# Optimization experiments

Hardware: AMD Instinct MI355X
Metric: run time of the kernel (lower is better)

## Reference

```python
import jax, jax.numpy as jnp
import numpy as np

N, E, D = 100000, 1280000, 64


def setup_inputs() -> dict:
    key = jax.random.key(0)
    ks = jax.random.split(key, 9)
    x = jax.random.normal(ks[0], (N, D), jnp.float32)
    edge_index = jax.random.randint(ks[1], (2, E), 0, N, dtype=jnp.int64)
    edge_weight = jax.random.uniform(ks[2], (E,), jnp.float32)
    s = 1.0 / np.sqrt(D)
    W0 = jax.random.normal(ks[3], (D, D), jnp.float32) * s
    b0 = jnp.zeros((D,), jnp.float32)
    W1 = jax.random.normal(ks[4], (D, D), jnp.float32) * s
    b1 = jnp.zeros((D,), jnp.float32)
    W2 = jax.random.normal(ks[5], (D, D), jnp.float32) * s
    b2 = jnp.zeros((D,), jnp.float32)
    return {"x": x, "edge_index": edge_index, "edge_weight": edge_weight,
            "W0": W0, "b0": b0, "W1": W1, "b1": b1, "W2": W2, "b2": b2}


def reference(x, edge_index, edge_weight, W0, b0, W1, b1, W2, b2):
    n = x.shape[0]
    row, col = edge_index[0], edge_index[1]
    # GCN normalization with self-loops (PyG gcn_norm, fill_value=1)
    loop = jnp.arange(n)
    row_f = jnp.concatenate([row, loop])
    col_f = jnp.concatenate([col, loop])
    w_f = jnp.concatenate([edge_weight, jnp.ones((n,), x.dtype)])
    deg = jax.ops.segment_sum(w_f, col_f, num_segments=n)
    dinv = jnp.where(deg > 0, jax.lax.rsqrt(deg), 0.0).astype(x.dtype)
    norm = dinv[row_f] * w_f * dinv[col_f]  # [E+N]

    def conv(h, W, b):
        h = h @ W                                  # [N, D_out]
        msg = h[row_f] * norm[:, None]             # gather + scale
        return jax.ops.segment_sum(msg, col_f, num_segments=n) + b

    results = [x]
    h = jax.nn.relu(conv(x, W0, b0))   # dropout p=0 / eval -> identity
    results.append(h)
    h = jax.nn.relu(conv(h, W1, b1))
    results.append(h)
    h = conv(h, W2, b2)                # last layer: no activation
    results.append(h)
    return tuple(results)
```

## Files before the change

kernel.cpp:

```cpp
#include <hip/hip_runtime.h>


#define TPB 256
#define P1_CHUNK 8192
#define DSH 7
#define DNB 128
#define STAGE_CAP 4096

__global__ __launch_bounds__(TPB) void k_p0(const int* __restrict__ col,
                                            int* __restrict__ chist, int E, int nbk) {
    __shared__ int h[1024];
    int tid = threadIdx.x;
    for (int i = tid; i < nbk; i += TPB) h[i] = 0;
    __syncthreads();
    int s0 = blockIdx.x * P1_CHUNK;
    int s1 = min(s0 + P1_CHUNK, E);
    for (int i = s0 + tid; i < s1; i += TPB) atomicAdd(&h[col[i] >> DSH], 1);
    __syncthreads();
    for (int i = tid; i < nbk; i += TPB)
        if (h[i]) atomicAdd(&chist[i], h[i]);
}

__global__ __launch_bounds__(1024) void k_scanb(const int* __restrict__ chist,
                                                int* __restrict__ cbase,
                                                int* __restrict__ ccur, int nbk, int E) {
    __shared__ int s[1024];
    int tid = threadIdx.x;
    int v = (tid < nbk) ? chist[tid] : 0;
    s[tid] = v;
    __syncthreads();
    for (int off = 1; off < 1024; off <<= 1) {
        int t = (tid >= off) ? s[tid - off] : 0;
        __syncthreads();
        s[tid] += t;
        __syncthreads();
    }
    if (tid < nbk) { int ex = s[tid] - v; cbase[tid] = ex; ccur[tid] = ex; }
    if (tid == 0) cbase[nbk] = E;
}

__global__ __launch_bounds__(TPB) void k_p1(const int* __restrict__ row,
                                            const int* __restrict__ col,
                                            const float* __restrict__ w,
                                            int* __restrict__ ccur,
                                            int2* __restrict__ bkt, int E, int nbk) {
    __shared__ int h[1024];
    __shared__ int base[1024];
    int tid = threadIdx.x;
    for (int i = tid; i < nbk; i += TPB) h[i] = 0;
    __syncthreads();
    int s0 = blockIdx.x * P1_CHUNK;
    int s1 = min(s0 + P1_CHUNK, E);
    for (int i = s0 + tid; i < s1; i += TPB) atomicAdd(&h[col[i] >> DSH], 1);
    __syncthreads();
    for (int i = tid; i < nbk; i += TPB) {
        int c = h[i];
        base[i] = c ? atomicAdd(&ccur[i], c) : 0;
        h[i] = 0;
    }
    __syncthreads();
    for (int i = s0 + tid; i < s1; i += TPB) {
        int c = col[i];
        int b = c >> DSH;
        int r = atomicAdd(&h[b], 1);
        bkt[base[b] + r] = make_int2(row[i] | ((c & (DNB - 1)) << 20), __float_as_int(w[i]));
    }
}

__global__ __launch_bounds__(TPB) void k_p2(const int2* __restrict__ bkt,
                                            const int* __restrict__ cbase,
                                            int* __restrict__ starts,
                                            int2* __restrict__ edges,
                                            float* __restrict__ dinv, int n, int E) {
    __shared__ int hist[DNB];
    __shared__ int curs[DNB];
    __shared__ int sc[DNB];
    __shared__ int2 stage[STAGE_CAP];
    int tid = threadIdx.x;
    int b = blockIdx.x;
    int s0 = cbase[b], s1 = cbase[b + 1];
    int cnt = s1 - s0;
    int nodeBase = b << DSH;
    if (tid < DNB) hist[tid] = 0;
    __syncthreads();
    for (int i = s0 + tid; i < s1; i += TPB)
        atomicAdd(&hist[(unsigned)bkt[i].x >> 20], 1);
    __syncthreads();
    int v = 0;
    if (tid < DNB) { v = hist[tid]; sc[tid] = v; }
    __syncthreads();
    for (int off = 1; off < DNB; off <<= 1) {
        int t = 0;
        if (tid < DNB && tid >= off) t = sc[tid - off];
        __syncthreads();
        if (tid < DNB) sc[tid] += t;
        __syncthreads();
    }
    if (tid < DNB) {
        int ex = sc[tid] - v;
        curs[tid] = ex;
        int node = nodeBase + tid;
        if (node < n) starts[node] = s0 + ex;
    }
    if (b == 0 && tid == 0) starts[n] = E;
    __syncthreads();
    if (cnt <= STAGE_CAP) {
        for (int i = s0 + tid; i < s1; i += TPB) {
            int2 ed = bkt[i];
            int d = (unsigned)ed.x >> 20;
            int r = atomicAdd(&curs[d], 1);
            stage[r] = make_int2(ed.x & 0xFFFFF, ed.y);
        }
        __syncthreads();
        for (int i = tid; i < cnt; i += TPB) edges[s0 + i] = stage[i];
        if (tid < DNB) {
            int node = nodeBase + tid;
            if (node < n) {
                float d = 1.0f;
                for (int j = sc[tid] - v; j < sc[tid]; ++j)
                    d += __int_as_float(stage[j].y);
                dinv[node] = rsqrtf(d);
            }
        }
    } else {
        for (int i = s0 + tid; i < s1; i += TPB) {
            int2 ed = bkt[i];
            int d = (unsigned)ed.x >> 20;
            int r = atomicAdd(&curs[d], 1);
            edges[s0 + r] = make_int2(ed.x & 0xFFFFF, ed.y);
        }
        __syncthreads();
        if (tid < DNB) {
            int node = nodeBase + tid;
            if (node < n) {
                float d = 1.0f;
                for (int j = sc[tid] - v; j < sc[tid]; ++j)
                    d += __int_as_float(edges[s0 + j].y);
                dinv[node] = rsqrtf(d);
            }
        }
    }
}

__global__ __launch_bounds__(TPB, 3) void k_gemm64(const float* __restrict__ in,
                                                   const float* __restrict__ Wg,
                                                   float* __restrict__ out,
                                                   float* __restrict__ cp, int n) {
    __shared__ float4 Ws[1024];
    __shared__ float4 As[2048];
    int tid = threadIdx.x;
    const float4* Wf4 = (const float4*)Wg;
    #pragma unroll
    for (int i = 0; i < 4; ++i) Ws[i * 256 + tid] = Wf4[i * 256 + tid];
    int rowbase = blockIdx.x * 128;
    const float4* Af4 = (const float4*)in;
    #pragma unroll
    for (int i = 0; i < 8; ++i) {
        int f4 = i * 256 + tid;
        int r = f4 >> 4, c4 = f4 & 15;
        float4 v = make_float4(0.f, 0.f, 0.f, 0.f);
        if (rowbase + r < n) {
            v = Af4[(size_t)(rowbase + r) * 16 + c4];
            if (cp) *(float4*)&cp[((size_t)(rowbase + r) * 16 + c4) * 4] = v;
        }
        As[r * 16 + (c4 ^ ((r >> 3) & 3))] = v;
    }
    __syncthreads();
    int jg = tid & 15;
    int rg = tid >> 4;
    int r0 = rg * 8;
    int sw = rg & 3;
    float4 acc[8];
    #pragma unroll
    for (int rr = 0; rr < 8; ++rr) acc[rr] = make_float4(0.f, 0.f, 0.f, 0.f);
    #pragma unroll 2
    for (int kt = 0; kt < 16; ++kt) {
        float4 w0 = Ws[(kt * 4 + 0) * 16 + jg];
        float4 w1 = Ws[(kt * 4 + 1) * 16 + jg];
        float4 w2 = Ws[(kt * 4 + 2) * 16 + jg];
        float4 w3 = Ws[(kt * 4 + 3) * 16 + jg];
        int ac = kt ^ sw;
        #pragma unroll
        for (int rr = 0; rr < 8; ++rr) {
            float4 a = As[(r0 + rr) * 16 + ac];
            acc[rr].x = fmaf(a.x, w0.x, acc[rr].x);
            acc[rr].y = fmaf(a.x, w0.y, acc[rr].y);
            acc[rr].z = fmaf(a.x, w0.z, acc[rr].z);
            acc[rr].w = fmaf(a.x, w0.w, acc[rr].w);
            acc[rr].x = fmaf(a.y, w1.x, acc[rr].x);
            acc[rr].y = fmaf(a.y, w1.y, acc[rr].y);
            acc[rr].z = fmaf(a.y, w1.z, acc[rr].z);
            acc[rr].w = fmaf(a.y, w1.w, acc[rr].w);
            acc[rr].x = fmaf(a.z, w2.x, acc[rr].x);
            acc[rr].y = fmaf(a.z, w2.y, acc[rr].y);
            acc[rr].z = fmaf(a.z, w2.z, acc[rr].z);
            acc[rr].w = fmaf(a.z, w2.w, acc[rr].w);
            acc[rr].x = fmaf(a.w, w3.x, acc[rr].x);
            acc[rr].y = fmaf(a.w, w3.y, acc[rr].y);
            acc[rr].z = fmaf(a.w, w3.z, acc[rr].z);
            acc[rr].w = fmaf(a.w, w3.w, acc[rr].w);
        }
    }
    #pragma unroll
    for (int rr = 0; rr < 8; ++rr) {
        int r = rowbase + r0 + rr;
        if (r < n) *(float4*)&out[(size_t)r * 64 + jg * 4] = acc[rr];
    }
}

__global__ __launch_bounds__(TPB) void k_gather(const int* __restrict__ starts,
                                                const int2* __restrict__ edges,
                                                const float* __restrict__ hw,
                                                const float* __restrict__ dinv,
                                                const float* __restrict__ b,
                                                float* __restrict__ out,
                                                int n, int relu) {
    int node = blockIdx.x * 4 + (threadIdx.x >> 6);
    if (node >= n) return;
    int lane = threadIdx.x & 63;
    int eslot = lane >> 4;
    int f = (lane & 15) << 2;
    int s0 = starts[node], s1 = starts[node + 1];
    float4 acc = make_float4(0.f, 0.f, 0.f, 0.f);
    int e = s0 + eslot;
    for (; e + 4 < s1; e += 8) {
        int2 ed0 = edges[e];
        int2 ed1 = edges[e + 4];
        float nm0 = dinv[ed0.x] * __int_as_float(ed0.y);
        float nm1 = dinv[ed1.x] * __int_as_float(ed1.y);
        float4 h0 = *(const float4*)&hw[(size_t)ed0.x * 64 + f];
        float4 h1 = *(const float4*)&hw[(size_t)ed1.x * 64 + f];
        acc.x = fmaf(h0.x, nm0, acc.x);
        acc.y = fmaf(h0.y, nm0, acc.y);
        acc.z = fmaf(h0.z, nm0, acc.z);
        acc.w = fmaf(h0.w, nm0, acc.w);
        acc.x = fmaf(h1.x, nm1, acc.x);
        acc.y = fmaf(h1.y, nm1, acc.y);
        acc.z = fmaf(h1.z, nm1, acc.z);
        acc.w = fmaf(h1.w, nm1, acc.w);
    }
    if (e < s1) {
        int2 ed = edges[e];
        float nm = dinv[ed.x] * __int_as_float(ed.y);
        float4 h = *(const float4*)&hw[(size_t)ed.x * 64 + f];
        acc.x = fmaf(h.x, nm, acc.x);
        acc.y = fmaf(h.y, nm, acc.y);
        acc.z = fmaf(h.z, nm, acc.z);
        acc.w = fmaf(h.w, nm, acc.w);
    }
    acc.x += __shfl_xor(acc.x, 16);
    acc.y += __shfl_xor(acc.y, 16);
    acc.z += __shfl_xor(acc.z, 16);
    acc.w += __shfl_xor(acc.w, 16);
    acc.x += __shfl_xor(acc.x, 32);
    acc.y += __shfl_xor(acc.y, 32);
    acc.z += __shfl_xor(acc.z, 32);
    acc.w += __shfl_xor(acc.w, 32);
    if (eslot == 0) {
        float di = dinv[node];
        float4 hs = *(const float4*)&hw[(size_t)node * 64 + f];
        float4 bb = *(const float4*)&b[f];
        float ix = fmaf(hs.x, di, acc.x);
        float iy = fmaf(hs.y, di, acc.y);
        float iz = fmaf(hs.z, di, acc.z);
        float iw = fmaf(hs.w, di, acc.w);
        float4 o;
        o.x = fmaf(ix, di, bb.x);
        o.y = fmaf(iy, di, bb.y);
        o.z = fmaf(iz, di, bb.z);
        o.w = fmaf(iw, di, bb.w);
        if (relu) {
            o.x = o.x > 0.f ? o.x : 0.f;
            o.y = o.y > 0.f ? o.y : 0.f;
            o.z = o.z > 0.f ? o.z : 0.f;
            o.w = o.w > 0.f ? o.w : 0.f;
        }
        *(float4*)&out[(size_t)node * 64 + f] = o;
    }
}

extern "C" void kernel_launch(void* const* d_in, const int* in_sizes, int n_in,
                              void* d_out, int out_size, void* d_ws, size_t ws_size,
                              hipStream_t stream) {
    const float* x = (const float*)d_in[0];
    const int* ei = (const int*)d_in[1];
    const float* ew = (const float*)d_in[2];
    const float* Wl[3] = {(const float*)d_in[3], (const float*)d_in[5], (const float*)d_in[7]};
    const float* Bl[3] = {(const float*)d_in[4], (const float*)d_in[6], (const float*)d_in[8]};

    const int n = in_sizes[0] / 64;
    const int E = in_sizes[2];
    const int* row = ei;
    const int* col = ei + E;
    float* out = (float*)d_out;

    const int nbk = (n + DNB - 1) >> DSH;
    const int p1b = (E + P1_CHUNK - 1) / P1_CHUNK;

    char* ws = (char*)d_ws;
    size_t o = 0;
    float* dinv  = (float*)(ws + o);  o = (o + (size_t)n * 4 + 255) & ~(size_t)255;
    float* hw    = (float*)(ws + o);
    int2*  bkt   = (int2*)(ws + o);   o = (o + (size_t)n * 256 + 255) & ~(size_t)255;
    int* starts  = (int*)(ws + o);    o = (o + (size_t)(n + 1) * 4 + 255) & ~(size_t)255;
    int* chist   = (int*)(ws + o);    o = (o + 1024 * 4 + 255) & ~(size_t)255;
    int* cbase   = (int*)(ws + o);    o = (o + 1025 * 4 + 255) & ~(size_t)255;
    int* ccur    = (int*)(ws + o);    o = (o + 1024 * 4 + 255) & ~(size_t)255;
    int2* edges  = (int2*)(ws + o);

    hipMemsetAsync(chist, 0, (size_t)nbk * 4, stream);
    k_p0<<<p1b, TPB, 0, stream>>>(col, chist, E, nbk);
    k_scanb<<<1, 1024, 0, stream>>>(chist, cbase, ccur, nbk, E);
    k_p1<<<p1b, TPB, 0, stream>>>(row, col, ew, ccur, bkt, E, nbk);
    k_p2<<<nbk, TPB, 0, stream>>>(bkt, cbase, starts, edges, dinv, n, E);

    const float* hin = x;
    for (int L = 0; L < 3; ++L) {
        float* oseg = out + (size_t)(L + 1) * n * 64;
        k_gemm64<<<(n + 127) / 128, TPB, 0, stream>>>(hin, Wl[L], hw, L == 0 ? out : nullptr, n);
        k_gather<<<(n + 3) / 4, TPB, 0, stream>>>(starts, edges, hw, dinv, Bl[L], oseg, n, L < 2 ? 1 : 0);
        hin = oseg;
    }
}
```

Before: 434.0 us.

## Store pre-scaled GEMM output in fp16 and drop per-edge dinv gather

The GEMM now multiplies each output row by its dinv and writes it as fp16. That halves the size of the feature table the gather kernel reads at random. It also removes the per-edge dinv[src] lookup, because the source normalization is already folded into the stored features. Edge records are read with nontemporal 64-bit loads, and the P1 chunk size is halved. The cost is precision: intermediate features are rounded to fp16, which may exceed the tolerance.

```diff
diff --git a/kernel.cpp b/kernel.cpp
--- a/kernel.cpp
+++ b/kernel.cpp
@@ -1,8 +1,9 @@
 #include <hip/hip_runtime.h>
+#include <hip/hip_fp16.h>
 
 
 #define TPB 256
-#define P1_CHUNK 8192
+#define P1_CHUNK 4096
 #define DSH 7
 #define DNB 128
 #define STAGE_CAP 4096
@@ -144,7 +145,8 @@
 
 __global__ __launch_bounds__(TPB, 3) void k_gemm64(const float* __restrict__ in,
                                                    const float* __restrict__ Wg,
-                                                   float* __restrict__ out,
+                                                   __half* __restrict__ hwh,
+                                                   const float* __restrict__ dinvg,
                                                    float* __restrict__ cp, int n) {
     __shared__ float4 Ws[1024];
     __shared__ float4 As[2048];
@@ -204,13 +206,21 @@
     #pragma unroll
     for (int rr = 0; rr < 8; ++rr) {
         int r = rowbase + r0 + rr;
-        if (r < n) *(float4*)&out[(size_t)r * 64 + jg * 4] = acc[rr];
+        if (r < n) {
+            float di = dinvg[r];
+            ushort4 s;
+            s.x = __half_as_ushort(__float2half(acc[rr].x * di));
+            s.y = __half_as_ushort(__float2half(acc[rr].y * di));
+            s.z = __half_as_ushort(__float2half(acc[rr].z * di));
+            s.w = __half_as_ushort(__float2half(acc[rr].w * di));
+            *(ushort4*)&hwh[(size_t)r * 64 + jg * 4] = s;
+        }
     }
 }
 
 __global__ __launch_bounds__(TPB) void k_gather(const int* __restrict__ starts,
                                                 const int2* __restrict__ edges,
-                                                const float* __restrict__ hw,
+                                                const __half* __restrict__ hwh,
                                                 const float* __restrict__ dinv,
                                                 const float* __restrict__ b,
                                                 float* __restrict__ out,
@@ -222,31 +232,32 @@
     int f = (lane & 15) << 2;
     int s0 = starts[node], s1 = starts[node + 1];
     float4 acc = make_float4(0.f, 0.f, 0.f, 0.f);
+    const long long* epk = (const long long*)edges;
     int e = s0 + eslot;
     for (; e + 4 < s1; e += 8) {
-        int2 ed0 = edges[e];
-        int2 ed1 = edges[e + 4];
-        float nm0 = dinv[ed0.x] * __int_as_float(ed0.y);
-        float nm1 = dinv[ed1.x] * __int_as_float(ed1.y);
-        float4 h0 = *(const float4*)&hw[(size_t)ed0.x * 64 + f];
-        float4 h1 = *(const float4*)&hw[(size_t)ed1.x * 64 + f];
-        acc.x = fmaf(h0.x, nm0, acc.x);
-        acc.y = fmaf(h0.y, nm0, acc.y);
-        acc.z = fmaf(h0.z, nm0, acc.z);
-        acc.w = fmaf(h0.w, nm0, acc.w);
-        acc.x = fmaf(h1.x, nm1, acc.x);
-        acc.y = fmaf(h1.y, nm1, acc.y);
-        acc.z = fmaf(h1.z, nm1, acc.z);
-        acc.w = fmaf(h1.w, nm1, acc.w);
+        long long ev0 = __builtin_nontemporal_load(&epk[e]);
+        long long ev1 = __builtin_nontemporal_load(&epk[e + 4]);
+        ushort4 u0 = *(const ushort4*)&hwh[(size_t)(int)ev0 * 64 + f];
+        ushort4 u1 = *(const ushort4*)&hwh[(size_t)(int)ev1 * 64 + f];
+        float w0 = __int_as_float((int)(ev0 >> 32));
+        float w1 = __int_as_float((int)(ev1 >> 32));
+        acc.x = fmaf(__half2float(__ushort_as_half(u0.x)), w0, acc.x);
+        acc.y = fmaf(__half2float(__ushort_as_half(u0.y)), w0, acc.y);
+        acc.z = fmaf(__half2float(__ushort_as_half(u0.z)), w0, acc.z);
+        acc.w = fmaf(__half2float(__ushort_as_half(u0.w)), w0, acc.w);
+        acc.x = fmaf(__half2float(__ushort_as_half(u1.x)), w1, acc.x);
+        acc.y = fmaf(__half2float(__ushort_as_half(u1.y)), w1, acc.y);
+        acc.z = fmaf(__half2float(__ushort_as_half(u1.z)), w1, acc.z);
+        acc.w = fmaf(__half2float(__ushort_as_half(u1.w)), w1, acc.w);
     }
     if (e < s1) {
-        int2 ed = edges[e];
-        float nm = dinv[ed.x] * __int_as_float(ed.y);
-        float4 h = *(const float4*)&hw[(size_t)ed.x * 64 + f];
-        acc.x = fmaf(h.x, nm, acc.x);
-        acc.y = fmaf(h.y, nm, acc.y);
-        acc.z = fmaf(h.z, nm, acc.z);
-        acc.w = fmaf(h.w, nm, acc.w);
+        long long ev = __builtin_nontemporal_load(&epk[e]);
+        ushort4 u = *(const ushort4*)&hwh[(size_t)(int)ev * 64 + f];
+        float w = __int_as_float((int)(ev >> 32));
+        acc.x = fmaf(__half2float(__ushort_as_half(u.x)), w, acc.x);
+        acc.y = fmaf(__half2float(__ushort_as_half(u.y)), w, acc.y);
+        acc.z = fmaf(__half2float(__ushort_as_half(u.z)), w, acc.z);
+        acc.w = fmaf(__half2float(__ushort_as_half(u.w)), w, acc.w);
     }
     acc.x += __shfl_xor(acc.x, 16);
     acc.y += __shfl_xor(acc.y, 16);
@@ -258,17 +269,13 @@
     acc.w += __shfl_xor(acc.w, 32);
     if (eslot == 0) {
         float di = dinv[node];
-        float4 hs = *(const float4*)&hw[(size_t)node * 64 + f];
+        ushort4 us = *(const ushort4*)&hwh[(size_t)node * 64 + f];
         float4 bb = *(const float4*)&b[f];
-        float ix = fmaf(hs.x, di, acc.x);
-        float iy = fmaf(hs.y, di, acc.y);
-        float iz = fmaf(hs.z, di, acc.z);
-        float iw = fmaf(hs.w, di, acc.w);
         float4 o;
-        o.x = fmaf(ix, di, bb.x);
-        o.y = fmaf(iy, di, bb.y);
-        o.z = fmaf(iz, di, bb.z);
-        o.w = fmaf(iw, di, bb.w);
+        o.x = fmaf(__half2float(__ushort_as_half(us.x)) + acc.x, di, bb.x);
+        o.y = fmaf(__half2float(__ushort_as_half(us.y)) + acc.y, di, bb.y);
+        o.z = fmaf(__half2float(__ushort_as_half(us.z)) + acc.z, di, bb.z);
+        o.w = fmaf(__half2float(__ushort_as_half(us.w)) + acc.w, di, bb.w);
         if (relu) {
             o.x = o.x > 0.f ? o.x : 0.f;
             o.y = o.y > 0.f ? o.y : 0.f;
@@ -300,8 +307,12 @@
     char* ws = (char*)d_ws;
     size_t o = 0;
     float* dinv  = (float*)(ws + o);  o = (o + (size_t)n * 4 + 255) & ~(size_t)255;
-    float* hw    = (float*)(ws + o);
-    int2*  bkt   = (int2*)(ws + o);   o = (o + (size_t)n * 256 + 255) & ~(size_t)255;
+    __half* hwh  = (__half*)(ws + o);
+    int2*  bkt   = (int2*)(ws + o);
+    {
+        size_t hb = (size_t)n * 128, bb = (size_t)E * 8;
+        o = (o + (hb > bb ? hb : bb) + 255) & ~(size_t)255;
+    }
     int* starts  = (int*)(ws + o);    o = (o + (size_t)(n + 1) * 4 + 255) & ~(size_t)255;
     int* chist   = (int*)(ws + o);    o = (o + 1024 * 4 + 255) & ~(size_t)255;
     int* cbase   = (int*)(ws + o);    o = (o + 1025 * 4 + 255) & ~(size_t)255;
@@ -317,8 +328,8 @@
     const float* hin = x;
     for (int L = 0; L < 3; ++L) {
         float* oseg = out + (size_t)(L + 1) * n * 64;
-        k_gemm64<<<(n + 127) / 128, TPB, 0, stream>>>(hin, Wl[L], hw, L == 0 ? out : nullptr, n);
-        k_gather<<<(n + 3) / 4, TPB, 0, stream>>>(starts, edges, hw, dinv, Bl[L], oseg, n, L < 2 ? 1 : 0);
+        k_gemm64<<<(n + 127) / 128, TPB, 0, stream>>>(hin, Wl[L], hwh, dinv, L == 0 ? out : nullptr, n);
+        k_gather<<<(n + 3) / 4, TPB, 0, stream>>>(starts, edges, hwh, dinv, Bl[L], oseg, n, L < 2 ? 1 : 0);
         hin = oseg;
     }
 }
```

After: 424.4 us. -2.2%, faster.
